# Optimization experiments

Hardware: AMD Instinct MI355X
Metric: run time of the kernel (lower is better)

Reference implementation:

```python
import jax, jax.numpy as jnp
import numpy as np

D, D_r, G, I = 1024, 64, 2, 2
Ng = D // G  # 512
F = (2 * I + 1) * G  # 10 gathered features per group
BATCH = 4096


def _make_idx():
    # Replicates the torch index construction (modulo-wrapped ring neighbors).
    base = 2 * (np.arange(-I, I + 1).reshape(-1, 1) % Ng)  # (2I+1, 1)
    base = np.concatenate([base, base + 1], axis=1).reshape(-1)  # (2*(2I+1),) == (F,)
    idx = np.stack([(base + 2 * i) % D for i in range(Ng)], axis=0)  # (Ng, F)
    return jnp.asarray(idx, dtype=jnp.int64)


def setup_inputs() -> dict:
    key = jax.random.key(0)
    k1, k2, k3, k4 = jax.random.split(key, 4)
    x = jax.random.normal(k1, (BATCH, D), dtype=jnp.float32)
    # torch.nn.Linear init scale ~ 1/sqrt(fan_in)
    W_in = jax.random.normal(k2, (D_r, F), dtype=jnp.float32) / np.sqrt(F)
    b_in = jax.random.normal(k3, (D_r,), dtype=jnp.float32) / np.sqrt(F)
    W_out = jax.random.normal(k4, (G, D_r), dtype=jnp.float32) / np.sqrt(D_r)
    return {"x": x, "W_in": W_in, "b_in": b_in, "W_out": W_out, "idx": _make_idx()}


def reference(x, W_in, b_in, W_out, idx):
    # gather ring neighbors: [B, Ng, F]
    g = x[..., idx]
    # inner linear + tanh: [B, Ng, D_r]
    h = jnp.tanh(jnp.einsum('bnf,rf->bnr', g, W_in) + b_in)
    # outer linear (no bias): [B, Ng, G] -> reshape to [B, D]
    y = jnp.einsum('bnr,gr->bng', h, W_out).reshape(x.shape)
    return x + y
```

## Files before the change

kernel.cpp:

```cpp
#include <hip/hip_runtime.h>

typedef __fp16 half8   __attribute__((ext_vector_type(8)));
typedef __fp16 half2v  __attribute__((ext_vector_type(2)));
typedef float  float4v __attribute__((ext_vector_type(4)));

#define SCALE 2.88539008177792681f

#if defined(__has_builtin) && __has_builtin(__builtin_amdgcn_fdot2)
#define DOT2(a, b, c) __builtin_amdgcn_fdot2((a), (b), (c), false)
#else
#define DOT2(a, b, c) ((c) + (float)(a).x * (float)(b).x + (float)(a).y * (float)(b).y)
#endif

__global__ __launch_bounds__(256) void pe_mfma2(
    const float* __restrict__ x, const float* __restrict__ W_in,
    const float* __restrict__ b_in, const float* __restrict__ W_out,
    float* __restrict__ out, int batch)
{
    __shared__ __align__(16) float sx[2][1056];
    __shared__ __align__(16) float sWin[640];
    __shared__ __align__(16) float sWout[128];
    __shared__ __align__(16) float sb[64];

    const int t    = threadIdx.x;
    const int lane = t & 63;
    const int wv   = t >> 6;
    const int col  = lane & 15;
    const int quad = lane >> 4;
    const int row0 = 2 * blockIdx.x;
    const int nrows = (batch - row0 >= 2) ? 2 : 1;

    {
        const float* xr0 = x + (size_t)row0 * 1024;
        float4 v0 = reinterpret_cast<const float4*>(xr0)[t];
        reinterpret_cast<float4*>(sx[0] + 4)[t] = v0;
        if (t < 4) { sx[0][t] = xr0[1020 + t]; sx[0][1028 + t] = xr0[t]; }
        if (t >= 8 && t < 32) { sx[0][1024 + t] = 0.f; sx[1][1024 + t] = 0.f; }
        if (nrows == 2) {
            const float* xr1 = xr0 + 1024;
            float4 v1 = reinterpret_cast<const float4*>(xr1)[t];
            reinterpret_cast<float4*>(sx[1] + 4)[t] = v1;
            if (t < 4) { sx[1][t] = xr1[1020 + t]; sx[1][1028 + t] = xr1[t]; }
        }
    }
    if (t < 160)
        reinterpret_cast<float4*>(sWin)[t] = reinterpret_cast<const float4*>(W_in)[t];
    else if (t >= 192 && t < 224)
        reinterpret_cast<float4*>(sWout)[t - 192] = reinterpret_cast<const float4*>(W_out)[t - 192];
    else if (t >= 224 && t < 240)
        reinterpret_cast<float4*>(sb)[t - 224] = reinterpret_cast<const float4*>(b_in)[t - 224];
    __syncthreads();

    half8  Af[4];
    float4v Cb[4];
    half2v Wp[4][2][2];
    #pragma unroll
    for (int t4 = 0; t4 < 4; ++t4) {
        const int r = 16 * t4 + col;
        #pragma unroll
        for (int j = 0; j < 8; ++j) {
            const int k = 8 * quad + j;
            Af[t4][j] = (__fp16)((k < 10) ? sWin[r * 10 + k] * SCALE : 0.f);
        }
        const int rb = 16 * t4 + 4 * quad;
        #pragma unroll
        for (int e = 0; e < 4; ++e) Cb[t4][e] = sb[rb + e] * SCALE;
        #pragma unroll
        for (int p = 0; p < 2; ++p) {
            const int r0 = rb + 2 * p;
            #pragma unroll
            for (int g = 0; g < 2; ++g)
                Wp[t4][p][g] = __builtin_amdgcn_cvt_pkrtz(sWout[g * 64 + r0], sWout[g * 64 + r0 + 1]);
        }
    }

    for (int row = 0; row < nrows; ++row) {
        const float* sxr = sx[row];
        float* orow = out + (size_t)(row0 + row) * 1024;

        #pragma unroll 2
        for (int it = 0; it < 8; ++it) {
            const int tile = wv * 8 + it;
            const int n    = tile * 16 + col;
            const int base = 2 * n + 8 * quad;

            half8 Bf;
            #pragma unroll
            for (int p = 0; p < 4; ++p) {
                const float2 xv = *reinterpret_cast<const float2*>(sxr + base + 2 * p);
                const half2v h = __builtin_amdgcn_cvt_pkrtz(xv.x, xv.y);
                Bf[2 * p]     = h.x;
                Bf[2 * p + 1] = h.y;
            }

            float4v D[4];
            #pragma unroll
            for (int t4 = 0; t4 < 4; ++t4)
                D[t4] = __builtin_amdgcn_mfma_f32_16x16x32_f16(Af[t4], Bf, Cb[t4], 0, 0, 0);

            float g0 = 0.f, g1 = 0.f;
            #pragma unroll
            for (int t4 = 0; t4 < 4; ++t4) {
                float th[4];
                #pragma unroll
                for (int e = 0; e < 4; ++e) {
                    const float ex = __builtin_amdgcn_exp2f(D[t4][e]);
                    th[e] = fmaf(-2.f, __builtin_amdgcn_rcpf(1.f + ex), 1.f);
                }
                const half2v y01 = __builtin_amdgcn_cvt_pkrtz(th[0], th[1]);
                const half2v y23 = __builtin_amdgcn_cvt_pkrtz(th[2], th[3]);
                g0 = DOT2(y01, Wp[t4][0][0], g0);
                g0 = DOT2(y23, Wp[t4][1][0], g0);
                g1 = DOT2(y01, Wp[t4][0][1], g1);
                g1 = DOT2(y23, Wp[t4][1][1], g1);
            }

            g0 += __shfl_xor(g0, 16, 64);
            g0 += __shfl_xor(g0, 32, 64);
            g1 += __shfl_xor(g1, 16, 64);
            g1 += __shfl_xor(g1, 32, 64);

            if (quad == 0) {
                const float2 xr = *reinterpret_cast<const float2*>(sxr + 4 + 2 * n);
                float2 o;
                o.x = xr.x + g0;
                o.y = xr.y + g1;
                *reinterpret_cast<float2*>(orow + 2 * n) = o;
            }
        }
    }
}

extern "C" void kernel_launch(void* const* d_in, const int* in_sizes, int n_in,
                              void* d_out, int out_size, void* d_ws, size_t ws_size,
                              hipStream_t stream) {
    const float* x     = (const float*)d_in[0];
    const float* W_in  = (const float*)d_in[1];
    const float* b_in  = (const float*)d_in[2];
    const float* W_out = (const float*)d_in[3];
    float* out = (float*)d_out;
    const int batch = in_sizes[0] / 1024;
    const int grid  = (batch + 1) / 2;
    pe_mfma2<<<grid, 256, 0, stream>>>(x, W_in, b_in, W_out, out, batch);
}
```

Measured before the change: 113.1 us.

## Switch to 32x32 MFMA, fold bias into K, and use fp16 polynomial tanh

Measured after the change: 103.7 us. 8.3% less time.

```diff
diff --git a/kernel.cpp b/kernel.cpp
--- a/kernel.cpp
+++ b/kernel.cpp
@@ -1,10 +1,8 @@
 #include <hip/hip_runtime.h>
 
-typedef __fp16 half8   __attribute__((ext_vector_type(8)));
-typedef __fp16 half2v  __attribute__((ext_vector_type(2)));
-typedef float  float4v __attribute__((ext_vector_type(4)));
-
-#define SCALE 2.88539008177792681f
+typedef __fp16 half8    __attribute__((ext_vector_type(8)));
+typedef __fp16 half2v   __attribute__((ext_vector_type(2)));
+typedef float  float16v __attribute__((ext_vector_type(16)));
 
 #if defined(__has_builtin) && __has_builtin(__builtin_amdgcn_fdot2)
 #define DOT2(a, b, c) __builtin_amdgcn_fdot2((a), (b), (c), false)
@@ -12,12 +10,12 @@
 #define DOT2(a, b, c) ((c) + (float)(a).x * (float)(b).x + (float)(a).y * (float)(b).y)
 #endif
 
-__global__ __launch_bounds__(256) void pe_mfma2(
+__global__ __launch_bounds__(256) void pe_mfma32(
     const float* __restrict__ x, const float* __restrict__ W_in,
     const float* __restrict__ b_in, const float* __restrict__ W_out,
     float* __restrict__ out, int batch)
 {
-    __shared__ __align__(16) float sx[2][1056];
+    __shared__ __align__(16) float sx[4][1056];
     __shared__ __align__(16) float sWin[640];
     __shared__ __align__(16) float sWout[128];
     __shared__ __align__(16) float sb[64];
@@ -25,102 +23,102 @@
     const int t    = threadIdx.x;
     const int lane = t & 63;
     const int wv   = t >> 6;
-    const int col  = lane & 15;
-    const int quad = lane >> 4;
-    const int row0 = 2 * blockIdx.x;
-    const int nrows = (batch - row0 >= 2) ? 2 : 1;
+    const int n32  = lane & 31;
+    const int g    = lane >> 5;
+    const int row0 = 4 * blockIdx.x;
+    const int nrows = (batch - row0 >= 4) ? 4 : (batch - row0);
 
-    {
-        const float* xr0 = x + (size_t)row0 * 1024;
-        float4 v0 = reinterpret_cast<const float4*>(xr0)[t];
-        reinterpret_cast<float4*>(sx[0] + 4)[t] = v0;
-        if (t < 4) { sx[0][t] = xr0[1020 + t]; sx[0][1028 + t] = xr0[t]; }
-        if (t >= 8 && t < 32) { sx[0][1024 + t] = 0.f; sx[1][1024 + t] = 0.f; }
-        if (nrows == 2) {
-            const float* xr1 = xr0 + 1024;
-            float4 v1 = reinterpret_cast<const float4*>(xr1)[t];
-            reinterpret_cast<float4*>(sx[1] + 4)[t] = v1;
-            if (t < 4) { sx[1][t] = xr1[1020 + t]; sx[1][1028 + t] = xr1[t]; }
-        }
+    for (int r = 0; r < nrows; ++r) {
+        const float* xr = x + (size_t)(row0 + r) * 1024;
+        reinterpret_cast<float4*>(sx[r] + 4)[t] = reinterpret_cast<const float4*>(xr)[t];
+        if (t < 4) { sx[r][t] = xr[1020 + t]; sx[r][1028 + t] = xr[t]; }
     }
     if (t < 160)
         reinterpret_cast<float4*>(sWin)[t] = reinterpret_cast<const float4*>(W_in)[t];
-    else if (t >= 192 && t < 224)
-        reinterpret_cast<float4*>(sWout)[t - 192] = reinterpret_cast<const float4*>(W_out)[t - 192];
-    else if (t >= 224 && t < 240)
-        reinterpret_cast<float4*>(sb)[t - 224] = reinterpret_cast<const float4*>(b_in)[t - 224];
+    else if (t >= 160 && t < 192)
+        reinterpret_cast<float4*>(sWout)[t - 160] = reinterpret_cast<const float4*>(W_out)[t - 160];
+    else if (t >= 192 && t < 208)
+        reinterpret_cast<float4*>(sb)[t - 192] = reinterpret_cast<const float4*>(b_in)[t - 192];
     __syncthreads();
 
-    half8  Af[4];
-    float4v Cb[4];
-    half2v Wp[4][2][2];
+    half8 Af[2];
     #pragma unroll
-    for (int t4 = 0; t4 < 4; ++t4) {
-        const int r = 16 * t4 + col;
+    for (int mf = 0; mf < 2; ++mf) {
+        const int R = 32 * mf + n32;
         #pragma unroll
         for (int j = 0; j < 8; ++j) {
-            const int k = 8 * quad + j;
-            Af[t4][j] = (__fp16)((k < 10) ? sWin[r * 10 + k] * SCALE : 0.f);
-        }
-        const int rb = 16 * t4 + 4 * quad;
-        #pragma unroll
-        for (int e = 0; e < 4; ++e) Cb[t4][e] = sb[rb + e] * SCALE;
-        #pragma unroll
-        for (int p = 0; p < 2; ++p) {
-            const int r0 = rb + 2 * p;
-            #pragma unroll
-            for (int g = 0; g < 2; ++g)
-                Wp[t4][p][g] = __builtin_amdgcn_cvt_pkrtz(sWout[g * 64 + r0], sWout[g * 64 + r0 + 1]);
+            const int k = 8 * g + j;
+            const float w = (k < 10) ? sWin[R * 10 + k] : (k == 10 ? sb[R] : 0.f);
+            Af[mf][j] = (__fp16)w;
         }
     }
+    half2v Wp[2][8][2];
+    #pragma unroll
+    for (int mf = 0; mf < 2; ++mf)
+        #pragma unroll
+        for (int p = 0; p < 8; ++p) {
+            const int R = 32 * mf + ((p & 1) << 1) + 8 * (p >> 1) + 4 * g;
+            #pragma unroll
+            for (int o = 0; o < 2; ++o)
+                Wp[mf][p][o] = __builtin_amdgcn_cvt_pkrtz(sWout[o * 64 + R], sWout[o * 64 + R + 1]);
+        }
+
+    const half2v C0 = {(__fp16)0.98931f,     (__fp16)0.98931f};
+    const half2v C1 = {(__fp16)-0.26964f,    (__fp16)-0.26964f};
+    const half2v C2 = {(__fp16)0.054759f,    (__fp16)0.054759f};
+    const half2v C3 = {(__fp16)-0.0057126f,  (__fp16)-0.0057126f};
+    const half2v C4 = {(__fp16)0.00022867f,  (__fp16)0.00022867f};
+    const half2v HI = {(__fp16)3.0f,  (__fp16)3.0f};
+    const half2v LO = {(__fp16)-3.0f, (__fp16)-3.0f};
+    const half2v ONE0 = {(__fp16)1.0f, (__fp16)0.0f};
+    const half2v ZER0 = {(__fp16)0.0f, (__fp16)0.0f};
+    const float16v Zacc = {};
 
     for (int row = 0; row < nrows; ++row) {
         const float* sxr = sx[row];
         float* orow = out + (size_t)(row0 + row) * 1024;
 
         #pragma unroll 2
-        for (int it = 0; it < 8; ++it) {
-            const int tile = wv * 8 + it;
-            const int n    = tile * 16 + col;
-            const int base = 2 * n + 8 * quad;
+        for (int it = 0; it < 4; ++it) {
+            const int tile = wv * 4 + it;
+            const int n    = tile * 32 + n32;
+            const int base = 2 * n + 8 * g;
 
+            half2v hp[4];
+            #pragma unroll
+            for (int p = 0; p < 4; ++p) {
+                const float2 q = *reinterpret_cast<const float2*>(sxr + base + 2 * p);
+                hp[p] = __builtin_amdgcn_cvt_pkrtz(q.x, q.y);
+            }
+            if (g) { hp[1] = ONE0; hp[2] = ZER0; hp[3] = ZER0; }
             half8 Bf;
             #pragma unroll
-            for (int p = 0; p < 4; ++p) {
-                const float2 xv = *reinterpret_cast<const float2*>(sxr + base + 2 * p);
-                const half2v h = __builtin_amdgcn_cvt_pkrtz(xv.x, xv.y);
-                Bf[2 * p]     = h.x;
-                Bf[2 * p + 1] = h.y;
-            }
-
-            float4v D[4];
-            #pragma unroll
-            for (int t4 = 0; t4 < 4; ++t4)
-                D[t4] = __builtin_amdgcn_mfma_f32_16x16x32_f16(Af[t4], Bf, Cb[t4], 0, 0, 0);
+            for (int p = 0; p < 4; ++p) { Bf[2 * p] = hp[p].x; Bf[2 * p + 1] = hp[p].y; }
 
             float g0 = 0.f, g1 = 0.f;
             #pragma unroll
-            for (int t4 = 0; t4 < 4; ++t4) {
-                float th[4];
+            for (int mf = 0; mf < 2; ++mf) {
+                const float16v D = __builtin_amdgcn_mfma_f32_32x32x16_f16(Af[mf], Bf, Zacc, 0, 0, 0);
                 #pragma unroll
-                for (int e = 0; e < 4; ++e) {
-                    const float ex = __builtin_amdgcn_exp2f(D[t4][e]);
-                    th[e] = fmaf(-2.f, __builtin_amdgcn_rcpf(1.f + ex), 1.f);
+                for (int p = 0; p < 8; ++p) {
+                    half2v zt = __builtin_amdgcn_cvt_pkrtz(D[2 * p], D[2 * p + 1]);
+                    zt = __builtin_elementwise_min(__builtin_elementwise_max(zt, LO), HI);
+                    const half2v z2 = zt * zt;
+                    half2v P = C4;
+                    P = P * z2 + C3;
+                    P = P * z2 + C2;
+                    P = P * z2 + C1;
+                    P = P * z2 + C0;
+                    const half2v th = zt * P;
+                    g0 = DOT2(th, Wp[mf][p][0], g0);
+                    g1 = DOT2(th, Wp[mf][p][1], g1);
                 }
-                const half2v y01 = __builtin_amdgcn_cvt_pkrtz(th[0], th[1]);
-                const half2v y23 = __builtin_amdgcn_cvt_pkrtz(th[2], th[3]);
-                g0 = DOT2(y01, Wp[t4][0][0], g0);
-                g0 = DOT2(y23, Wp[t4][1][0], g0);
-                g1 = DOT2(y01, Wp[t4][0][1], g1);
-                g1 = DOT2(y23, Wp[t4][1][1], g1);
             }
 
-            g0 += __shfl_xor(g0, 16, 64);
             g0 += __shfl_xor(g0, 32, 64);
-            g1 += __shfl_xor(g1, 16, 64);
             g1 += __shfl_xor(g1, 32, 64);
 
-            if (quad == 0) {
+            if (lane < 32) {
                 const float2 xr = *reinterpret_cast<const float2*>(sxr + 4 + 2 * n);
                 float2 o;
                 o.x = xr.x + g0;
@@ -140,6 +138,6 @@
     const float* W_out = (const float*)d_in[3];
     float* out = (float*)d_out;
     const int batch = in_sizes[0] / 1024;
-    const int grid  = (batch + 1) / 2;
-    pe_mfma2<<<grid, 256, 0, stream>>>(x, W_in, b_in, W_out, out, batch);
+    const int grid  = (batch + 3) / 4;
+    pe_mfma32<<<grid, 256, 0, stream>>>(x, W_in, b_in, W_out, out, batch);
 }
```
